# Kernel tuning notes

Measured on AMD Instinct MI355X. Metric: run time of the kernel, lower is better.

## Reference

```python
import jax, jax.numpy as jnp
import numpy as np

B, S, D = 2, 2048, 3584
H, KV, HD = 28, 4, 128
N_REP = H // KV          # 7
MAX_S = 2048
SCALE = HD ** -0.5
ROPE_BASE = 1_000_000.0  # Qwen2 rope theta


def _rope_tables(max_s, hd, base):
    inv = 1.0 / (base ** (np.arange(0, hd, 2, dtype=np.float32) / hd))  # [hd/2]
    ang = np.arange(max_s, dtype=np.float32)[:, None] * inv[None, :]    # [S, hd/2]
    return jnp.asarray(np.cos(ang)), jnp.asarray(np.sin(ang))


def apply_rotary(x, cos, sin):
    # x: [b, s, h, hd] with interleaved complex pairs (torch view_as_complex layout)
    xr = x[..., 0::2]
    xi = x[..., 1::2]
    cos = cos[None, :, None, :]
    sin = sin[None, :, None, :]
    yr = xr * cos - xi * sin
    yi = xr * sin + xi * cos
    return jnp.stack([yr, yi], axis=-1).reshape(x.shape)


def setup_inputs() -> dict:
    key = jax.random.key(0)
    ks = jax.random.split(key, 8)
    w = 0.02
    x = jax.random.normal(ks[0], (B, S, D), jnp.float32)
    wq_w = jax.random.normal(ks[1], (H * HD, D), jnp.float32) * w
    wq_b = jax.random.normal(ks[2], (H * HD,), jnp.float32) * w
    wk_w = jax.random.normal(ks[3], (KV * HD, D), jnp.float32) * w
    wk_b = jax.random.normal(ks[4], (KV * HD,), jnp.float32) * w
    wv_w = jax.random.normal(ks[5], (KV * HD, D), jnp.float32) * w
    wv_b = jax.random.normal(ks[6], (KV * HD,), jnp.float32) * w
    wo_w = jax.random.normal(ks[7], (D, H * HD), jnp.float32) * w
    k_cache = jnp.zeros((B, MAX_S, KV, HD), jnp.float32)
    v_cache = jnp.zeros((B, MAX_S, KV, HD), jnp.float32)
    freqs_cos, freqs_sin = _rope_tables(MAX_S, HD, ROPE_BASE)
    # causal additive mask [s, t]; large-negative instead of -inf for safe grads
    mask = jnp.triu(jnp.full((S, S), -1e9, jnp.float32), k=1)
    return {"x": x, "wq_w": wq_w, "wq_b": wq_b, "wk_w": wk_w, "wk_b": wk_b,
            "wv_w": wv_w, "wv_b": wv_b, "wo_w": wo_w,
            "k_cache": k_cache, "v_cache": v_cache,
            "freqs_cos": freqs_cos, "freqs_sin": freqs_sin,
            "mask": mask, "start_pos": 0}


def reference(x, wq_w, wq_b, wk_w, wk_b, wv_w, wv_b, wo_w,
              k_cache, v_cache, freqs_cos, freqs_sin, mask, start_pos):
    bsz, seqlen, _ = x.shape
    end_pos = start_pos + seqlen
    q = (x @ wq_w.T + wq_b).reshape(bsz, seqlen, H, HD)
    k = (x @ wk_w.T + wk_b).reshape(bsz, seqlen, KV, HD)
    v = (x @ wv_w.T + wv_b).reshape(bsz, seqlen, KV, HD)
    cos = jax.lax.dynamic_slice_in_dim(freqs_cos, start_pos, seqlen, 0)
    sin = jax.lax.dynamic_slice_in_dim(freqs_sin, start_pos, seqlen, 0)
    q = apply_rotary(q, cos, sin)
    k = apply_rotary(k, cos, sin)
    # KV-cache write
    k_cache = jax.lax.dynamic_update_slice(k_cache, k, (0, start_pos, 0, 0))
    v_cache = jax.lax.dynamic_update_slice(v_cache, v, (0, start_pos, 0, 0))
    keys = k_cache[:bsz, :end_pos]    # [b, t, kv, hd]
    values = v_cache[:bsz, :end_pos]
    # GQA: repeat_interleave kv heads to n_heads
    keys = jnp.repeat(keys, N_REP, axis=2)      # [b, t, h, hd]
    values = jnp.repeat(values, N_REP, axis=2)
    scores = jnp.einsum('bshd,bthd->bsht', q, keys) * SCALE
    scores = scores + mask[None, :, None, :]
    probs = jax.nn.softmax(scores.astype(jnp.float32), axis=-1).astype(x.dtype)
    out = jnp.einsum('bsht,bthd->bshd', probs, values)
    out = out.reshape(bsz, seqlen, H * HD)
    return out @ wo_w.T
```

## Files before the change

### kernel.cpp

```cpp
#include <hip/hip_runtime.h>
#include <hip/hip_bf16.h>

typedef __attribute__((ext_vector_type(4)))  float  f32x4;
typedef __attribute__((ext_vector_type(16))) float  f32x16;
typedef __attribute__((ext_vector_type(8)))  __bf16 bf16x8;
typedef __attribute__((ext_vector_type(4)))  __bf16 bf16x4;
typedef __attribute__((ext_vector_type(4)))  unsigned int u32x4;

constexpr int S_LEN = 2048, DMODEL = 3584, NH = 28, NKV = 4, HD = 128, NREP = 7;
constexpr float SCALE_LOG2 = 0.1275174331f;

__device__ __forceinline__ unsigned int pack2(float a, float b) {
  unsigned short ua = __builtin_bit_cast(unsigned short, (__bf16)a);
  unsigned short ub = __builtin_bit_cast(unsigned short, (__bf16)b);
  return (unsigned int)ua | ((unsigned int)ub << 16);
}

__global__ void cvt5_kernel(const float* __restrict__ s0, const float* __restrict__ s1,
                            const float* __restrict__ s2, const float* __restrict__ s3,
                            const float* __restrict__ s4,
                            __bf16* __restrict__ d0, __bf16* __restrict__ d1,
                            __bf16* __restrict__ d2, __bf16* __restrict__ d3,
                            __bf16* __restrict__ d4,
                            int n0, int n1, int n2, int n3, int* __restrict__ ctr, int total) {
  if (blockIdx.x == 0 && threadIdx.x == 0) *ctr = 0;
  for (int i = blockIdx.x * blockDim.x + threadIdx.x; i < total; i += gridDim.x * blockDim.x) {
    const float* s; __bf16* d; int j = i;
    if (j < n0) { s = s0; d = d0; }
    else { j -= n0;
      if (j < n1) { s = s1; d = d1; }
      else { j -= n1;
        if (j < n2) { s = s2; d = d2; }
        else { j -= n2;
          if (j < n3) { s = s3; d = d3; }
          else { j -= n3; s = s4; d = d4; }
        }
      }
    }
    float4 v = reinterpret_cast<const float4*>(s)[j];
    bf16x4 o;
    o[0] = (__bf16)v.x; o[1] = (__bf16)v.y; o[2] = (__bf16)v.z; o[3] = (__bf16)v.w;
    reinterpret_cast<bf16x4*>(d)[j] = o;
  }
}

#define GLDS16(gsrc, ldst)                                                              \
  __builtin_amdgcn_global_load_lds((const __attribute__((address_space(1))) void*)(gsrc),\
                                   (__attribute__((address_space(3))) void*)(ldst), 16, 0, 0)

template <int MODE>
__global__ __launch_bounds__(512, 2) void gemm256(
    const __bf16* __restrict__ A, const __bf16* __restrict__ Bw,
    const float* __restrict__ bias, void* __restrict__ Cout,
    int M, int N, int K,
    const float* __restrict__ fcos, const float* __restrict__ fsin,
    const int* __restrict__ sp_ptr, float scale)
{
  extern __shared__ char smem[];
  const int tid = threadIdx.x;
  const int lane = tid & 63, wid = tid >> 6;
  const int wm = wid >> 2, wn = wid & 3;
  const int l15 = lane & 15, g = (lane >> 4) & 3;

  const int chunk = gridDim.x >> 3;
  const int wg = (blockIdx.x & 7) * chunk + (blockIdx.x >> 3);
  const int nbx = N >> 8;
  const int by = wg / nbx, bx = wg % nbx;
  const int row0 = by * 256, col0 = bx * 256;

  const int srL   = 16 * (tid >> 6) + ((tid >> 2) & 15);
  const int cperm = ((tid & 3) * 8) ^ (((tid >> 5) & 1) * 16);
  const __bf16* pA0 = A + (size_t)(row0 + srL) * K + cperm;
  const __bf16* pA1 = pA0 + (size_t)128 * K;
  char* ldsA = smem + tid * 16;

  const int sw = ((l15 >> 3) & 1) << 5;
  const int aoff = wm * 8192 + l15 * 64 + ((g * 16) ^ sw);

  const __bf16* pBf[4];
#pragma unroll
  for (int fn = 0; fn < 4; fn++)
    pBf[fn] = Bw + (size_t)(col0 + wn * 64 + fn * 16 + l15) * K + g * 8;

  f32x4 acc[8][4] = {};
  const int nt = K >> 5;
  bf16x8 bE[4], bO[4];

#pragma unroll
  for (int pt = 0; pt < 3; pt++) {
    char* sA = ldsA + pt * 16384;
    GLDS16(pA0 + (size_t)pt * 32, sA);
    GLDS16(pA1 + (size_t)pt * 32, sA + 8192);
  }
  __builtin_amdgcn_sched_barrier(0);
#pragma unroll
  for (int fn = 0; fn < 4; fn++) bE[fn] = *reinterpret_cast<const bf16x8*>(pBf[fn]);
#pragma unroll
  for (int fn = 0; fn < 4; fn++) bO[fn] = *reinterpret_cast<const bf16x8*>(pBf[fn] + 32);
  asm volatile("s_waitcnt vmcnt(12)" ::: "memory");
  __builtin_amdgcn_s_barrier();
  __builtin_amdgcn_sched_barrier(0);

#define TILE(T, BR)                                                                     \
  do {                                                                                  \
    const int slot = ((T) & 3) * 16384;                                                 \
    const char* sa = smem + slot + aoff;                                                \
    bf16x8 a0[4], a1[4];                                                                \
    _Pragma("unroll")                                                                   \
    for (int fm = 0; fm < 4; fm++)                                                      \
      a0[fm] = *reinterpret_cast<const bf16x8*>(sa + fm * 1024);                        \
    _Pragma("unroll")                                                                   \
    for (int fm = 0; fm < 4; fm++)                                                      \
      a1[fm] = *reinterpret_cast<const bf16x8*>(sa + (4 + fm) * 1024);                  \
                         \
    if ((T) == 0)            asm volatile("s_waitcnt vmcnt(4) lgkmcnt(0)" ::: "memory");\
    else if ((T) <= nt - 3)  asm volatile("s_waitcnt vmcnt(6) lgkmcnt(0)" ::: "memory");\
    else if ((T) == nt - 2)  asm volatile("s_waitcnt vmcnt(4) lgkmcnt(0)" ::: "memory");\
    else                     asm volatile("s_waitcnt vmcnt(0) lgkmcnt(0)" ::: "memory");\
    __builtin_amdgcn_sched_barrier(0);                                                  \
    __builtin_amdgcn_s_setprio(1);                                                      \
    _Pragma("unroll")                                                                   \
    for (int fn = 0; fn < 4; fn++)                                                      \
      _Pragma("unroll")                                                                 \
      for (int fm = 0; fm < 4; fm++)                                                    \
        acc[fm][fn] = __builtin_amdgcn_mfma_f32_16x16x32_bf16(a0[fm], BR[fn],           \
                                                              acc[fm][fn], 0, 0, 0);   \
    _Pragma("unroll")                                                                   \
    for (int fn = 0; fn < 4; fn++)                                                      \
      _Pragma("unroll")                                                                 \
      for (int fm = 0; fm < 4; fm++)                                                    \
        acc[4 + fm][fn] = __builtin_amdgcn_mfma_f32_16x16x32_bf16(a1[fm], BR[fn],       \
                                                                  acc[4 + fm][fn],     \
                                                                  0, 0, 0);            \
    __builtin_amdgcn_s_setprio(0);                                                      \
    __builtin_amdgcn_sched_barrier(0);                                                  \
                \
    if ((T) + 3 < nt) {                                                                 \
      char* sA = ldsA + (((T) + 3) & 3) * 16384;                                        \
      GLDS16(pA0 + (size_t)((T) + 3) * 32, sA);                                         \
      GLDS16(pA1 + (size_t)((T) + 3) * 32, sA + 8192);                                  \
    }                                                                                   \
    if ((T) + 2 < nt) {                                                                 \
      _Pragma("unroll")                                                                 \
      for (int fn = 0; fn < 4; fn++)                                                    \
        BR[fn] = *reinterpret_cast<const bf16x8*>(pBf[fn] + (size_t)((T) + 2) * 32);    \
    }                                                                                   \
    __builtin_amdgcn_s_barrier();                                                       \
    __builtin_amdgcn_sched_barrier(0);                                                  \
  } while (0)

  for (int t = 0; t < nt; t += 2) {
    TILE(t, bE);
    TILE(t + 1, bO);
  }
#undef TILE

  if constexpr (MODE == 0) {
    float* C = (float*)Cout;
#pragma unroll
    for (int fm = 0; fm < 8; fm++) {
      const int row = row0 + wm * 128 + fm * 16 + 4 * g;
#pragma unroll
      for (int fn = 0; fn < 4; fn++) {
        const int col = col0 + wn * 64 + fn * 16 + l15;
#pragma unroll
        for (int r = 0; r < 4; r++)
          C[(size_t)(row + r) * N + col] = acc[fm][fn][r];
      }
    }
  } else {
    __bf16* C = (__bf16*)Cout;
    const int sp = sp_ptr[0];
    float bval[4];
#pragma unroll
    for (int fn = 0; fn < 4; fn++) bval[fn] = bias[col0 + wn * 64 + fn * 16 + l15];
#pragma unroll
    for (int fm = 0; fm < 8; fm++) {
#pragma unroll
      for (int fn = 0; fn < 4; fn++) {
        const int col = col0 + wn * 64 + fn * 16 + l15;
        const int i = (col & (HD - 1)) >> 1;
#pragma unroll
        for (int r = 0; r < 4; r++) {
          const int row = row0 + wm * 128 + fm * 16 + 4 * g + r;
          float y = acc[fm][fn][r] + bval[fn];
          float p = __shfl_xor(y, 1);
          const int spos = sp + (row & (S_LEN - 1));
          const float c = fcos[spos * (HD / 2) + i];
          const float sn = fsin[spos * (HD / 2) + i];
          y = (col & 1) ? (p * sn + y * c) : (y * c - p * sn);
          C[(size_t)row * N + col] = (__bf16)(y * scale);
        }
      }
    }
  }
}

__global__ __launch_bounds__(256) void gemm_kv(
    const __bf16* __restrict__ A,
    const __bf16* __restrict__ Wk, const float* __restrict__ bk, __bf16* __restrict__ Ko,
    const __bf16* __restrict__ Wv, const float* __restrict__ bv, __bf16* __restrict__ Vt,
    const float* __restrict__ fcos, const float* __restrict__ fsin,
    const int* __restrict__ sp_ptr)
{
  constexpr int N = 512, K = 3584;
  __shared__ __bf16 As[128 * 32];
  __shared__ __bf16 Bs[128 * 32];
  const int tid = threadIdx.x;
  const int lane = tid & 63, wid = tid >> 6;
  const int l15 = lane & 15, g = lane >> 4;
  const int wr = wid >> 1, wc = wid & 1;
  const bool isK = blockIdx.x < 4;
  const __bf16* Bw = isK ? Wk : Wv;
  const float* bias = isK ? bk : bv;
  const int row0 = blockIdx.y * 128;
  const int col0 = (blockIdx.x & 3) * 128;

  f32x4 acc[4][4] = {};

  const int srow = tid >> 2;
  const int scol = (tid & 3) * 8;
  const __bf16* Ag0 = A + (size_t)(row0 + srow) * K + scol;
  const __bf16* Ag1 = Ag0 + (size_t)64 * K;
  const __bf16* Bg0 = Bw + (size_t)(col0 + srow) * K + scol;
  const __bf16* Bg1 = Bg0 + (size_t)64 * K;
  __bf16* As0 = As + tid * 8;
  __bf16* As1 = As + 2048 + tid * 8;
  __bf16* Bs0 = Bs + tid * 8;
  __bf16* Bs1 = Bs + 2048 + tid * 8;

  for (int k0 = 0; k0 < K; k0 += 32) {
    GLDS16(Ag0 + k0, As0);
    GLDS16(Ag1 + k0, As1);
    GLDS16(Bg0 + k0, Bs0);
    GLDS16(Bg1 + k0, Bs1);
    __syncthreads();
    bf16x8 af[4], bfr[4];
#pragma unroll
    for (int m = 0; m < 4; m++)
      af[m] = *reinterpret_cast<const bf16x8*>(As + (wr * 64 + m * 16 + l15) * 32 + g * 8);
#pragma unroll
    for (int n = 0; n < 4; n++)
      bfr[n] = *reinterpret_cast<const bf16x8*>(Bs + (wc * 64 + n * 16 + l15) * 32 + g * 8);
#pragma unroll
    for (int m = 0; m < 4; m++)
#pragma unroll
      for (int n = 0; n < 4; n++)
        acc[m][n] = __builtin_amdgcn_mfma_f32_16x16x32_bf16(af[m], bfr[n], acc[m][n], 0, 0, 0);
    __syncthreads();
  }

  const int sp = sp_ptr[0];
  if (isK) {
#pragma unroll
    for (int m = 0; m < 4; m++) {
#pragma unroll
      for (int n = 0; n < 4; n++) {
        const int col = col0 + wc * 64 + n * 16 + l15;
        const float bval = bias[col];
        f32x4 v = acc[m][n];
#pragma unroll
        for (int r = 0; r < 4; r++) {
          const int row = row0 + wr * 64 + m * 16 + 4 * g + r;
          float y = v[r] + bval;
          float p = __shfl_xor(y, 1);
          const int i = (col & (HD - 1)) >> 1;
          const int spos = sp + (row & (S_LEN - 1));
          const float c = fcos[spos * (HD / 2) + i];
          const float sn = fsin[spos * (HD / 2) + i];
          y = (col & 1) ? (p * sn + y * c) : (y * c - p * sn);
          Ko[(size_t)row * N + col] = (__bf16)y;
        }
      }
    }
  } else {
    const int b4kv = ((row0 >> 11) * 4) + (blockIdx.x & 3);
    __bf16* vbase = Vt + ((size_t)b4kv << 18);
#pragma unroll
    for (int m = 0; m < 4; m++) {
#pragma unroll
      for (int n = 0; n < 4; n++) {
        const int d = wc * 64 + n * 16 + l15;
        const float bval = bias[col0 + d];
        const int s0 = (row0 + wr * 64 + m * 16 + 4 * g) & (S_LEN - 1);
        f32x4 v = acc[m][n];
        bf16x4 o;
#pragma unroll
        for (int r = 0; r < 4; r++) o[r] = (__bf16)(v[r] + bval);
        *reinterpret_cast<bf16x4*>(vbase + (size_t)d * S_LEN + s0) = o;
      }
    }
  }
}

__global__ __launch_bounds__(256, 2) void attn_kernel(
    const __bf16* __restrict__ Qb, const __bf16* __restrict__ Kb,
    const __bf16* __restrict__ Vt, __bf16* __restrict__ Ob, int* __restrict__ ctr)
{
  __shared__ __align__(16) char asmem[65536];
  __shared__ int jsh;

  const int tid = threadIdx.x, lane = tid & 63, wid = tid >> 6;
  const int l31 = lane & 31, hh = lane >> 5;

  const int trow = tid >> 4;
  const int kcol = (((tid & 15) * 16) ^ ((trow & 7) << 4)) >> 1;
  const int vrow = tid >> 3;
  const int vcol = (((tid & 7) * 16) ^ ((vrow & 7) << 4)) >> 1;

  constexpr int NITEMS = 16 * NH * 2;

  while (true) {
    if (tid == 0) jsh = atomicAdd(ctr, 1);
    __syncthreads();
    const int j = jsh;
    if (j >= NITEMS) break;

    const int qi = 15 - (j / 56);
    const int r56 = j % 56;
    const int h = r56 >> 1, b = r56 & 1;
    const int kvh = h / NREP;
    const int qw = qi * 128 + wid * 32;
    const int qg = qw + l31;

    const __bf16* Kbase = Kb + ((size_t)b * S_LEN * NKV + kvh) * HD;
    const __bf16* Vbase = Vt + ((size_t)b * NKV + kvh) * (size_t)HD * S_LEN;

    bf16x8 qf[8];
    {
      const __bf16* qp = Qb + (((size_t)b * S_LEN + qg) * NH + h) * HD + hh * 8;
#pragma unroll
      for (int c = 0; c < 8; c++) qf[c] = *reinterpret_cast<const bf16x8*>(qp + c * 16);
    }

    f32x16 o[4] = {};
    float mrun = -3.0e38f, lsum = 0.0f;

    const int ntiles = 2 * qi + 2;

#define STAGE(T, S)                                                                     \
    do {                                                                                \
      const int k0_ = (T) * 64;                                                         \
      char* Kd_ = asmem + (S) * 32768;                                                  \
      char* Vd_ = Kd_ + 16384;                                                          \
      _Pragma("unroll")                                                                 \
      for (int p = 0; p < 4; p++) {                                                     \
        GLDS16(Kbase + (size_t)(k0_ + p * 16 + trow) * (NKV * HD) + kcol,               \
               Kd_ + (p * 256 + tid) * 16);                                             \
        GLDS16(Vbase + (size_t)(p * 32 + vrow) * S_LEN + k0_ + vcol,                    \
               Vd_ + (p * 256 + tid) * 16);                                             \
      }                                                                                 \
    } while (0)

    STAGE(0, 0);

    for (int t = 0; t < ntiles; t++) {
      __syncthreads();
      if (t + 1 < ntiles) STAGE(t + 1, (t + 1) & 1);

      const char* Ksb = asmem + (t & 1) * 32768;
      const char* Vsb = Ksb + 16384;
      const int k0 = t * 64;

      f32x16 s0 = {}, s1 = {};
      {
        const char* kp0 = Ksb + l31 * 256;
        const char* kp1 = kp0 + 32 * 256;
        const int sw = (l31 & 7) << 4;
        __builtin_amdgcn_s_setprio(1);
#pragma unroll
        for (int c = 0; c < 8; c++) {
          const int cb = (c * 32 + hh * 16) ^ sw;
          bf16x8 kf0 = *reinterpret_cast<const bf16x8*>(kp0 + cb);
          s0 = __builtin_amdgcn_mfma_f32_32x32x16_bf16(kf0, qf[c], s0, 0, 0, 0);
          bf16x8 kf1 = *reinterpret_cast<const bf16x8*>(kp1 + cb);
          s1 = __builtin_amdgcn_mfma_f32_32x32x16_bf16(kf1, qf[c], s1, 0, 0, 0);
        }
        __builtin_amdgcn_s_setprio(0);
      }

      if (k0 + 63 > qw) {
#pragma unroll
        for (int r = 0; r < 16; r++) {
          const int kvo = k0 + ((r & 3) + 8 * (r >> 2)) + 4 * hh;
          if (kvo > qg)      s0[r] = -1.0e9f;
          if (kvo + 32 > qg) s1[r] = -1.0e9f;
        }
      }

      float pmax = -3.0e38f;
#pragma unroll
      for (int r = 0; r < 16; r++) { pmax = fmaxf(pmax, s0[r]); pmax = fmaxf(pmax, s1[r]); }
      pmax = fmaxf(pmax, __shfl_xor(pmax, 32));
      if (!__all(pmax <= mrun + 11.5f)) {
        const float mnew = fmaxf(mrun, pmax);
        const float fs = exp2f(mrun - mnew);
        lsum *= fs;
#pragma unroll
        for (int dt = 0; dt < 4; dt++) o[dt] *= fs;
        mrun = mnew;
      }
      float psum = 0.0f;
#pragma unroll
      for (int r = 0; r < 16; r++) {
        s0[r] = exp2f(s0[r] - mrun); psum += s0[r];
        s1[r] = exp2f(s1[r] - mrun); psum += s1[r];
      }
      lsum += psum;

      unsigned int pk[2][8], px[2][8];
#pragma unroll
      for (int jj = 0; jj < 8; jj++) {
        pk[0][jj] = pack2(s0[2 * jj], s0[2 * jj + 1]);
        pk[1][jj] = pack2(s1[2 * jj], s1[2 * jj + 1]);
      }
#pragma unroll
      for (int tt = 0; tt < 2; tt++)
#pragma unroll
        for (int jj = 0; jj < 8; jj++) px[tt][jj] = __shfl_xor(pk[tt][jj], 32);

      __builtin_amdgcn_s_setprio(1);
#pragma unroll
      for (int tt = 0; tt < 2; tt++) {
#pragma unroll
        for (int c2 = 0; c2 < 2; c2++) {
          u32x4 pb4;
          if (hh == 0)
            pb4 = (u32x4){pk[tt][4 * c2], pk[tt][4 * c2 + 1], px[tt][4 * c2], px[tt][4 * c2 + 1]};
          else
            pb4 = (u32x4){px[tt][4 * c2 + 2], px[tt][4 * c2 + 3], pk[tt][4 * c2 + 2], pk[tt][4 * c2 + 3]};
          bf16x8 pbf = __builtin_bit_cast(bf16x8, pb4);
          const int colb = tt * 64 + c2 * 32 + hh * 16;
#pragma unroll
          for (int dt = 0; dt < 4; dt++) {
            const int d = dt * 32 + l31;
            bf16x8 vf = *reinterpret_cast<const bf16x8*>(Vsb + d * 128 + (colb ^ ((d & 7) << 4)));
            o[dt] = __builtin_amdgcn_mfma_f32_32x32x16_bf16(vf, pbf, o[dt], 0, 0, 0);
          }
        }
      }
      __builtin_amdgcn_s_setprio(0);
    }
#undef STAGE

    lsum += __shfl_xor(lsum, 32);
    const float inv = 1.0f / lsum;
    char* my = asmem + wid * 8192;
#pragma unroll
    for (int dt = 0; dt < 4; dt++) {
#pragma unroll
      for (int jj = 0; jj < 8; jj++) {
        const int r = 2 * jj;
        const int d = dt * 32 + ((r & 3) + 8 * (r >> 2)) + 4 * hh;
        const unsigned int w = pack2(o[dt][r] * inv, o[dt][r + 1] * inv);
        *reinterpret_cast<unsigned int*>(my + ((l31 * 256 + d * 2) ^ ((l31 & 7) << 4))) = w;
      }
    }
#pragma unroll
    for (int jj = 0; jj < 8; jj++) {
      const int idx = jj * 64 + lane;
      const int row = idx >> 4, c16 = idx & 15;
      u32x4 val = *reinterpret_cast<u32x4*>(my + row * 256 + ((c16 * 16) ^ ((row & 7) << 4)));
      *reinterpret_cast<u32x4*>(Ob + (size_t)(b * S_LEN + qw + row) * (NH * HD) + h * HD + c16 * 8) = val;
    }
  }
}

extern "C" void kernel_launch(void* const* d_in, const int* in_sizes, int n_in,
                              void* d_out, int out_size, void* d_ws, size_t ws_size,
                              hipStream_t stream) {
  (void)in_sizes; (void)n_in; (void)out_size; (void)ws_size;
  const float* x    = (const float*)d_in[0];
  const float* wq_w = (const float*)d_in[1];
  const float* wq_b = (const float*)d_in[2];
  const float* wk_w = (const float*)d_in[3];
  const float* wk_b = (const float*)d_in[4];
  const float* wv_w = (const float*)d_in[5];
  const float* wv_b = (const float*)d_in[6];
  const float* wo_w = (const float*)d_in[7];
  const float* fcos = (const float*)d_in[10];
  const float* fsin = (const float*)d_in[11];
  const int*   spp  = (const int*)d_in[13];
  float* out = (float*)d_out;

  constexpr size_t XB_N = (size_t)4096 * 3584;
  constexpr size_t WQ_N = (size_t)3584 * 3584;
  constexpr size_t WK_N = (size_t)512 * 3584;
  constexpr size_t WO_N = (size_t)3584 * 3584;
  constexpr size_t KB_N = (size_t)4096 * 512;

  __bf16* xb  = (__bf16*)d_ws;
  __bf16* wqb = xb + XB_N;
  __bf16* wkb = wqb + WQ_N;
  __bf16* wvb = wkb + WK_N;
  __bf16* wob = wvb + WK_N;
  __bf16* Qb  = wob + WO_N;
  __bf16* Kb  = Qb + XB_N;
  __bf16* Vt  = Kb + KB_N;
  int*    ctr = (int*)(Vt + KB_N);
  __bf16* Ob  = xb;

  constexpr int N0 = (int)(XB_N / 4), N1 = (int)(WQ_N / 4), N2 = (int)(WK_N / 4),
                N3 = (int)(WK_N / 4), N4 = (int)(WO_N / 4);
  constexpr int NTOT = N0 + N1 + N2 + N3 + N4;
  cvt5_kernel<<<2048, 256, 0, stream>>>(x, wq_w, wk_w, wv_w, wo_w,
                                        xb, wqb, wkb, wvb, wob,
                                        N0, N1, N2, N3, ctr, NTOT);

  gemm256<2><<<dim3(224), 512, 65536, stream>>>(xb, wqb, wq_b, Qb, 4096, 3584, 3584,
                                                fcos, fsin, spp, SCALE_LOG2);
  gemm_kv<<<dim3(8, 32), 256, 0, stream>>>(xb, wkb, wk_b, Kb, wvb, wv_b, Vt,
                                           fcos, fsin, spp);
  attn_kernel<<<dim3(512), 256, 0, stream>>>(Qb, Kb, Vt, Ob, ctr);
  gemm256<0><<<dim3(224), 512, 65536, stream>>>(Ob, wob, nullptr, out, 4096, 3584, 3584,
                                                nullptr, nullptr, nullptr, 1.0f);
}
```

Measured before the change: 484.3 us.

## Stage GEMM B operand through LDS alongside A instead of direct global loads

The 256x256 GEMM used to stage only the A tile in LDS while each wave read its B fragments straight from global memory. Now both A and B tiles go through LDS via async global-to-LDS copies into a 4-slot ring, and B fragments for the next k-step are prefetched from LDS. The wait counts are reworked so the two MFMA halves overlap with LDS reads. This cuts redundant global B traffic across the wave rows, at the cost of doubling LDS to 128 KB per block, which may limit occupancy and add LDS bandwidth pressure.

```diff
diff --git a/kernel.cpp b/kernel.cpp
--- a/kernel.cpp
+++ b/kernel.cpp
@@ -72,15 +72,14 @@
   const int cperm = ((tid & 3) * 8) ^ (((tid >> 5) & 1) * 16);
   const __bf16* pA0 = A + (size_t)(row0 + srL) * K + cperm;
   const __bf16* pA1 = pA0 + (size_t)128 * K;
+  const __bf16* pB0 = Bw + (size_t)(col0 + srL) * K + cperm;
+  const __bf16* pB1 = pB0 + (size_t)128 * K;
   char* ldsA = smem + tid * 16;
+  char* ldsB = smem + 65536 + tid * 16;
 
   const int sw = ((l15 >> 3) & 1) << 5;
   const int aoff = wm * 8192 + l15 * 64 + ((g * 16) ^ sw);
-
-  const __bf16* pBf[4];
-#pragma unroll
-  for (int fn = 0; fn < 4; fn++)
-    pBf[fn] = Bw + (size_t)(col0 + wn * 64 + fn * 16 + l15) * K + g * 8;
+  const int boff = 65536 + wn * 4096 + l15 * 64 + ((g * 16) ^ sw);
 
   f32x4 acc[8][4] = {};
   const int nt = K >> 5;
@@ -88,23 +87,27 @@
 
 #pragma unroll
   for (int pt = 0; pt < 3; pt++) {
+    const size_t ko = (size_t)pt * 32;
     char* sA = ldsA + pt * 16384;
-    GLDS16(pA0 + (size_t)pt * 32, sA);
-    GLDS16(pA1 + (size_t)pt * 32, sA + 8192);
-  }
-  __builtin_amdgcn_sched_barrier(0);
-#pragma unroll
-  for (int fn = 0; fn < 4; fn++) bE[fn] = *reinterpret_cast<const bf16x8*>(pBf[fn]);
-#pragma unroll
-  for (int fn = 0; fn < 4; fn++) bO[fn] = *reinterpret_cast<const bf16x8*>(pBf[fn] + 32);
-  asm volatile("s_waitcnt vmcnt(12)" ::: "memory");
+    char* sB = ldsB + pt * 16384;
+    GLDS16(pA0 + ko, sA);
+    GLDS16(pA1 + ko, sA + 8192);
+    GLDS16(pB0 + ko, sB);
+    GLDS16(pB1 + ko, sB + 8192);
+  }
+  asm volatile("s_waitcnt vmcnt(4)" ::: "memory");
   __builtin_amdgcn_s_barrier();
   __builtin_amdgcn_sched_barrier(0);
-
-#define TILE(T, BR)                                                                     \
+  {
+    const char* sb0 = smem + boff;
+#pragma unroll
+    for (int fn = 0; fn < 4; fn++)
+      bE[fn] = *reinterpret_cast<const bf16x8*>(sb0 + fn * 1024);
+  }
+
+#define GTILE(T, BC, BN)                                                                \
   do {                                                                                  \
-    const int slot = ((T) & 3) * 16384;                                                 \
-    const char* sa = smem + slot + aoff;                                                \
+    const char* sa = smem + ((T) & 3) * 16384 + aoff;                                   \
     bf16x8 a0[4], a1[4];                                                                \
     _Pragma("unroll")                                                                   \
     for (int fm = 0; fm < 4; fm++)                                                      \
@@ -112,48 +115,55 @@
     _Pragma("unroll")                                                                   \
     for (int fm = 0; fm < 4; fm++)                                                      \
       a1[fm] = *reinterpret_cast<const bf16x8*>(sa + (4 + fm) * 1024);                  \
-                         \
-    if ((T) == 0)            asm volatile("s_waitcnt vmcnt(4) lgkmcnt(0)" ::: "memory");\
-    else if ((T) <= nt - 3)  asm volatile("s_waitcnt vmcnt(6) lgkmcnt(0)" ::: "memory");\
-    else if ((T) == nt - 2)  asm volatile("s_waitcnt vmcnt(4) lgkmcnt(0)" ::: "memory");\
-    else                     asm volatile("s_waitcnt vmcnt(0) lgkmcnt(0)" ::: "memory");\
+    const bool hasnext = (T) + 1 < nt;                                                  \
+    if (hasnext) {                                                                      \
+      const char* sbn = smem + (((T) + 1) & 3) * 16384 + boff;                          \
+      _Pragma("unroll")                                                                 \
+      for (int fn = 0; fn < 4; fn++)                                                    \
+        BN[fn] = *reinterpret_cast<const bf16x8*>(sbn + fn * 1024);                     \
+    }                                                                                   \
+    if ((T) + 3 < nt) {         \
+      const size_t ko = (size_t)((T) + 3) * 32;                                         \
+      char* sA = ldsA + (((T) + 3) & 3) * 16384;                                        \
+      char* sB = ldsB + (((T) + 3) & 3) * 16384;                                        \
+      GLDS16(pA0 + ko, sA);                                                             \
+      GLDS16(pA1 + ko, sA + 8192);                                                      \
+      GLDS16(pB0 + ko, sB);                                                             \
+      GLDS16(pB1 + ko, sB + 8192);                                                      \
+    }                                                                                   \
+    asm volatile("s_waitcnt lgkmcnt(8)" ::: "memory");                                  \
     __builtin_amdgcn_sched_barrier(0);                                                  \
     __builtin_amdgcn_s_setprio(1);                                                      \
     _Pragma("unroll")                                                                   \
     for (int fn = 0; fn < 4; fn++)                                                      \
       _Pragma("unroll")                                                                 \
       for (int fm = 0; fm < 4; fm++)                                                    \
-        acc[fm][fn] = __builtin_amdgcn_mfma_f32_16x16x32_bf16(a0[fm], BR[fn],           \
+        acc[fm][fn] = __builtin_amdgcn_mfma_f32_16x16x32_bf16(a0[fm], BC[fn],           \
                                                               acc[fm][fn], 0, 0, 0);   \
+    __builtin_amdgcn_s_setprio(0);                                                      \
+    if (hasnext) asm volatile("s_waitcnt lgkmcnt(4)" ::: "memory");                     \
+    else         asm volatile("s_waitcnt lgkmcnt(0)" ::: "memory");                     \
+    __builtin_amdgcn_sched_barrier(0);                                                  \
+    __builtin_amdgcn_s_setprio(1);                                                      \
     _Pragma("unroll")                                                                   \
     for (int fn = 0; fn < 4; fn++)                                                      \
       _Pragma("unroll")                                                                 \
       for (int fm = 0; fm < 4; fm++)                                                    \
-        acc[4 + fm][fn] = __builtin_amdgcn_mfma_f32_16x16x32_bf16(a1[fm], BR[fn],       \
+        acc[4 + fm][fn] = __builtin_amdgcn_mfma_f32_16x16x32_bf16(a1[fm], BC[fn],       \
                                                                   acc[4 + fm][fn],     \
                                                                   0, 0, 0);            \
     __builtin_amdgcn_s_setprio(0);                                                      \
-    __builtin_amdgcn_sched_barrier(0);                                                  \
-                \
-    if ((T) + 3 < nt) {                                                                 \
-      char* sA = ldsA + (((T) + 3) & 3) * 16384;                                        \
-      GLDS16(pA0 + (size_t)((T) + 3) * 32, sA);                                         \
-      GLDS16(pA1 + (size_t)((T) + 3) * 32, sA + 8192);                                  \
-    }                                                                                   \
-    if ((T) + 2 < nt) {                                                                 \
-      _Pragma("unroll")                                                                 \
-      for (int fn = 0; fn < 4; fn++)                                                    \
-        BR[fn] = *reinterpret_cast<const bf16x8*>(pBf[fn] + (size_t)((T) + 2) * 32);    \
-    }                                                                                   \
+    if ((T) < nt - 3) asm volatile("s_waitcnt vmcnt(4)" ::: "memory");                  \
+    else              asm volatile("s_waitcnt vmcnt(0)" ::: "memory");                  \
     __builtin_amdgcn_s_barrier();                                                       \
     __builtin_amdgcn_sched_barrier(0);                                                  \
   } while (0)
 
   for (int t = 0; t < nt; t += 2) {
-    TILE(t, bE);
-    TILE(t + 1, bO);
-  }
-#undef TILE
+    GTILE(t, bE, bO);
+    GTILE(t + 1, bO, bE);
+  }
+#undef GTILE
 
   if constexpr (MODE == 0) {
     float* C = (float*)Cout;
@@ -507,11 +517,11 @@
                                         xb, wqb, wkb, wvb, wob,
                                         N0, N1, N2, N3, ctr, NTOT);
 
-  gemm256<2><<<dim3(224), 512, 65536, stream>>>(xb, wqb, wq_b, Qb, 4096, 3584, 3584,
-                                                fcos, fsin, spp, SCALE_LOG2);
+  gemm256<2><<<dim3(224), 512, 131072, stream>>>(xb, wqb, wq_b, Qb, 4096, 3584, 3584,
+                                                 fcos, fsin, spp, SCALE_LOG2);
   gemm_kv<<<dim3(8, 32), 256, 0, stream>>>(xb, wkb, wk_b, Kb, wvb, wv_b, Vt,
                                            fcos, fsin, spp);
   attn_kernel<<<dim3(512), 256, 0, stream>>>(Qb, Kb, Vt, Ob, ctr);
-  gemm256<0><<<dim3(224), 512, 65536, stream>>>(Ob, wob, nullptr, out, 4096, 3584, 3584,
-                                                nullptr, nullptr, nullptr, 1.0f);
+  gemm256<0><<<dim3(224), 512, 131072, stream>>>(Ob, wob, nullptr, out, 4096, 3584, 3584,
+                                                 nullptr, nullptr, nullptr, 1.0f);
 }
```

Result: faster. 422.2 us (-12.8%).
